# Performance work log

Hardware: AMD Instinct MI355X
Metric: run time of the kernel (lower is better)

## Reference

```python
import jax, jax.numpy as jnp
from jax import lax
import numpy as np

BN_EPS = 1e-3


def _bn_train(x, gamma, beta):
    # training-mode BatchNorm2d: batch stats over (N, H, W), biased variance
    mean = jnp.mean(x, axis=(0, 2, 3), keepdims=True)
    var = jnp.var(x, axis=(0, 2, 3), keepdims=True)
    g = gamma[None, :, None, None]
    b = beta[None, :, None, None]
    return (x - mean) * lax.rsqrt(var + BN_EPS) * g + b


def _pointwise(x, w, b, gamma, beta):
    # 1x1 conv + BN + relu (reluM = clamp(min=0))
    y = jnp.einsum('bchw,oc->bohw', x, w) + b[None, :, None, None]
    return jnp.maximum(_bn_train(y, gamma, beta), 0.0)


def _depthwise1d(x, w, b, gamma, beta):
    # depthwise (1,5) conv, zero pad width by 2 each side, BN, clamp(-8,8)
    C = w.shape[0]
    k = w[:, None, None, :]  # [C,1,1,5]
    y = lax.conv_general_dilated(
        x, k, window_strides=(1, 1), padding=[(0, 0), (2, 2)],
        feature_group_count=C,
        dimension_numbers=('NCHW', 'OIHW', 'NCHW'))
    y = y + b[None, :, None, None]
    return jnp.clip(_bn_train(y, gamma, beta), -8.0, 8.0)


def _iir(x, w3, gamma, beta):
    # y[0] = (a+b+c)*x[0];  y[r] = a*x[r] + b*x[r-1] + c*y[r-1]
    a = w3[0][:, None]  # w_curr_inp, [C,1]
    b = w3[1][:, None]  # w_prev_inp
    c = w3[2][:, None]  # w_prev_out
    xT = jnp.moveaxis(x, 2, 0)  # [H,B,C,W]
    y0 = (a + b + c) * xT[0]

    def step(y_prev, xs):
        x_curr, x_prev = xs
        y = a * x_curr + b * x_prev + c * y_prev
        return y, y

    _, ys = lax.scan(step, y0, (xT[1:], xT[:-1]))
    y = jnp.concatenate([y0[None], ys], axis=0)
    y = jnp.moveaxis(y, 0, 2)  # back to [B,C,H,W]
    return jnp.clip(_bn_train(y, gamma, beta), -8.0, 8.0)


def _process_unit(x, u, iir_w, iir_gamma, iir_beta, dw_w, dw_b, dw_gamma,
                  dw_beta, pw_w, pw_b, pw_gamma, pw_beta):
    h = _iir(x, iir_w[u], iir_gamma[u], iir_beta[u])
    h = _depthwise1d(h, dw_w[u], dw_b[u], dw_gamma[u], dw_beta[u])
    return _pointwise(h, pw_w[u], pw_b[u], pw_gamma[u], pw_beta[u])


def setup_inputs() -> dict:
    key = jax.random.key(0)
    ks = jax.random.split(key, 16)
    B, Cin, Cout, H, W = 4, 36, 72, 256, 256
    return {
        'x': jax.random.normal(ks[0], (B, Cin, H, W), jnp.float32),
        'expand_w': jax.random.normal(ks[1], (Cout, Cin), jnp.float32),
        'expand_b': jax.random.normal(ks[2], (Cout,), jnp.float32),
        'expand_gamma': jax.random.uniform(ks[3], (Cout,), jnp.float32),
        'expand_beta': jax.random.normal(ks[4], (Cout,), jnp.float32),
        'iir_w': jax.random.uniform(ks[5], (4, 3, Cout), jnp.float32),
        'iir_gamma': jax.random.uniform(ks[6], (4, Cout), jnp.float32),
        'iir_beta': jax.random.normal(ks[7], (4, Cout), jnp.float32),
        'dw_w': jax.random.normal(ks[8], (4, Cout, 5), jnp.float32),
        'dw_b': jax.random.normal(ks[9], (4, Cout), jnp.float32),
        'dw_gamma': jax.random.uniform(ks[10], (4, Cout), jnp.float32),
        'dw_beta': jax.random.normal(ks[11], (4, Cout), jnp.float32),
        'pw_w': jax.random.normal(ks[12], (4, Cout, Cout), jnp.float32),
        'pw_b': jax.random.normal(ks[13], (4, Cout), jnp.float32),
        'pw_gamma': jax.random.uniform(ks[14], (4, Cout), jnp.float32),
        'pw_beta': jax.random.normal(ks[15], (4, Cout), jnp.float32),
    }


def reference(x, expand_w, expand_b, expand_gamma, expand_beta, iir_w,
              iir_gamma, iir_beta, dw_w, dw_b, dw_gamma, dw_beta, pw_w,
              pw_b, pw_gamma, pw_beta):
    h = _pointwise(x, expand_w, expand_b, expand_gamma, expand_beta)
    unit = lambda z, u: _process_unit(z, u, iir_w, iir_gamma, iir_beta, dw_w,
                                      dw_b, dw_gamma, dw_beta, pw_w, pw_b,
                                      pw_gamma, pw_beta)
    h = h + unit(unit(h, 0), 1)
    h = h + unit(unit(h, 2), 3)
    return h
```

## Files before the change

### kernel.cpp

```cpp
#include <hip/hip_runtime.h>
#include <hip/hip_fp16.h>

#define BBATCH 4
#define CCH 72
#define HROW 256
#define WCOL 256
#define HWSZ (HROW*WCOL)
#define NPC (BBATCH*HROW*WCOL)
#define BNEPS 1e-3f
#define NSH 64
#define SST 144

typedef unsigned short u16;
typedef unsigned int u32;
typedef _Float16 h8 __attribute__((ext_vector_type(8)));
typedef float f32x4 __attribute__((ext_vector_type(4)));

__device__ __forceinline__ float h2f(u16 h_){ return __half2float(__ushort_as_half(h_)); }
__device__ __forceinline__ u16 f2h(float f){ return __half_as_ushort(__float2half(f)); }
__device__ __forceinline__ u32 pack2(float a, float b){ return (u32)f2h(a) | ((u32)f2h(b)<<16); }
__device__ __forceinline__ float clip8(float v){ return fminf(fmaxf(v,-8.f),8.f); }

__device__ __forceinline__ void get_ss_wave(int c, int lane, const float* __restrict__ pstat,
                                            const float* __restrict__ gam, const float* __restrict__ bet,
                                            float& sc, float& sh){
  float s = pstat[lane*SST + c];
  float q = pstat[lane*SST + 72 + c];
  #pragma unroll
  for (int off=32; off; off>>=1){ s += __shfl_xor(s,off); q += __shfl_xor(q,off); }
  float mean = s * (1.0f/(float)NPC);
  float var  = q * (1.0f/(float)NPC) - mean*mean;
  sc = gam[c] * rsqrtf(var + BNEPS);
  sh = bet[c] - mean*sc;
}

__global__ __launch_bounds__(256) void k_prep(const float* __restrict__ ew,
    const float* __restrict__ pwall, u16* __restrict__ Wp)
{
  for (int e = blockIdx.x*256 + threadIdx.x; e < 14*3200; e += gridDim.x*256){
    int slab = e / 3200, rem = e - slab*3200;
    int row = rem / 40, col = rem - row*40;
    float w = 0.f;
    if (slab < 2){
      int c = slab*32 + col;
      if (row < 72 && col < 32 && c < 36) w = ew[row*36 + c];
    } else {
      int u = (slab-2)/3, kb = (slab-2)%3;
      int c = kb*32 + col;
      if (row < 72 && col < 32) w = pwall[u*5184 + row*72 + c];
    }
    Wp[e] = f2h(w);
  }
}

template<int CIN, int RAW>
__global__ __launch_bounds__(512) void k_pw(const void* __restrict__ in_,
    u16* __restrict__ out, const u16* __restrict__ Wp,
    const float* __restrict__ pstat,
    const float* __restrict__ pgam, const float* __restrict__ pbet,
    float* __restrict__ ostat)
{
  constexpr int KB = (CIN + 31) / 32;
  __shared__ __align__(16) u16 xs[72*264];
  __shared__ float tsc[80], tsh[80];
  __shared__ float sst[72], sqt[72];
  float* pp4 = (float*)xs;
  float* pq4 = pp4 + 320;

  const int tid  = threadIdx.x;
  const int lane = tid & 63;
  const int wid  = tid >> 6;
  const int g    = lane >> 4;
  const int li   = lane & 15;
  const int b    = blockIdx.x >> 8;
  const int hrow = blockIdx.x & 255;

  if (tid < 72){ sst[tid] = 0.f; sqt[tid] = 0.f; }

  if constexpr (!RAW){
    int sg = tid >> 7, c = tid & 127;
    if (c < 72){
      float s = 0.f, q = 0.f;
      #pragma unroll
      for (int k2 = 0; k2 < 16; ++k2){
        s += pstat[(sg*16 + k2)*SST + c];
        q += pstat[(sg*16 + k2)*SST + 72 + c];
      }
      pp4[sg*80 + c] = s; pq4[sg*80 + c] = q;
    }
    __syncthreads();
    if (tid < CIN){
      float s = pp4[tid] + pp4[80+tid] + pp4[160+tid] + pp4[240+tid];
      float q = pq4[tid] + pq4[80+tid] + pq4[160+tid] + pq4[240+tid];
      float mean = s * (1.0f/(float)NPC);
      float var  = q * (1.0f/(float)NPC) - mean*mean;
      float scv  = pgam[tid] * rsqrtf(var + BNEPS);
      tsc[tid] = scv;
      tsh[tid] = pbet[tid] - mean*scv;
    }
    __syncthreads();
  }

  const size_t base_in = (size_t)b*CIN*HWSZ + (size_t)hrow*WCOL;
  const int px0 = wid*32 + li;
  f32x4 acc[5][2];
  #pragma unroll
  for (int mt=0; mt<5; ++mt){ acc[mt][0] = (f32x4){0,0,0,0}; acc[mt][1] = (f32x4){0,0,0,0}; }

  #pragma unroll
  for (int kb2 = 0; kb2 < KB; ++kb2){
    h8 bf0, bf1;
    #pragma unroll
    for (int j = 0; j < 8; ++j){
      int c  = kb2*32 + g*8 + j;
      int cc = (c < CIN) ? c : 0;
      float v0, v1;
      if constexpr (RAW){
        const float* ip = (const float*)in_ + base_in + (size_t)cc*HWSZ;
        v0 = ip[px0]; v1 = ip[px0 + 16];
      } else {
        const u16* ip = (const u16*)in_ + base_in + (size_t)cc*HWSZ;
        float scv = tsc[cc], shv = tsh[cc];
        v0 = clip8(h2f(ip[px0])*scv + shv);
        v1 = clip8(h2f(ip[px0 + 16])*scv + shv);
      }
      bool ok = (c < CIN);
      bf0[j] = (_Float16)(ok ? v0 : 0.f);
      bf1[j] = (_Float16)(ok ? v1 : 0.f);
    }
    #pragma unroll
    for (int mt = 0; mt < 5; ++mt){
      h8 ah = *(const h8*)(Wp + (size_t)(kb2*80 + mt*16 + li)*40 + g*8);
      acc[mt][0] = __builtin_amdgcn_mfma_f32_16x16x32_f16(ah, bf0, acc[mt][0], 0, 0, 0);
      acc[mt][1] = __builtin_amdgcn_mfma_f32_16x16x32_f16(ah, bf1, acc[mt][1], 0, 0, 0);
    }
  }

  #pragma unroll
  for (int mt = 0; mt < 5; ++mt){
    int o = mt*16 + g*4;
    if (o < 72){
      #pragma unroll
      for (int t2 = 0; t2 < 2; ++t2){
        int px = wid*32 + t2*16 + li;
        #pragma unroll
        for (int r = 0; r < 4; ++r)
          xs[(o + r)*264 + px] = f2h(acc[mt][t2][r]);
      }
    }
  }
  __syncthreads();

  #pragma unroll
  for (int it = 0; it < 5; ++it){
    int e = tid + it*512;
    if (e < 72*32){
      int o = e >> 5, m = e & 31;
      uint4 v = *(const uint4*)&xs[o*264 + m*8];
      u32 rr[4] = {v.x, v.y, v.z, v.w};
      float s = 0.f, q = 0.f;
      #pragma unroll
      for (int q2=0; q2<4; ++q2){
        float a  = h2f((u16)rr[q2]);
        float bq = h2f((u16)(rr[q2]>>16));
        s += a + bq;
        q = fmaf(a,a,q); q = fmaf(bq,bq,q);
      }
      *(uint4*)(out + (size_t)b*CCH*HWSZ + (size_t)o*HWSZ + (size_t)hrow*WCOL + m*8) = v;
      #pragma unroll
      for (int off = 1; off <= 16; off <<= 1){ s += __shfl_xor(s, off); q += __shfl_xor(q, off); }
      if ((lane & 31) == 0){ atomicAdd(&sst[o], s); atomicAdd(&sqt[o], q); }
    }
  }
  __syncthreads();
  if (tid < 72){
    float* oshard = ostat + (size_t)(blockIdx.x & (NSH-1))*SST;
    atomicAdd(oshard + tid,      sst[tid]);
    atomicAdd(oshard + 72 + tid, sqt[tid]);
  }
}

template<int MODE>
__global__ __launch_bounds__(256) void k_iir(const u16* __restrict__ in, u16* __restrict__ out,
    const float* __restrict__ wabc, u16* __restrict__ hbuf,
    const float* __restrict__ pstat,
    const float* __restrict__ pgam, const float* __restrict__ pbet,
    float* __restrict__ ostat)
{
  const int tid = threadIdx.x;
  const int bc = blockIdx.x;
  const int c = bc % CCH;
  float sc, sh; get_ss_wave(c, tid&63, pstat, pgam, pbet, sc, sh);
  const float ka = wabc[c], kb = wabc[CCH+c], kcc = wabc[2*CCH+c];
  const size_t base = (size_t)bc*HWSZ + tid;
  float xprev=0.f, yprev=0.f, lsum=0.f, lssq=0.f;

  float a0[16], a1[16], r0[16], r1[16];

  auto LOADC = [&](int hb, float* xv, float* rv){
    #pragma unroll
    for (int j=0;j<16;++j){
      size_t idx = base + (size_t)(hb+j)*WCOL;
      xv[j] = h2f(in[idx]);
      if (MODE==2) rv[j] = h2f(hbuf[idx]);
    }
  };
  auto COMPC = [&](int hb, const float* xv, const float* rv){
    float x[16];
    #pragma unroll
    for (int j=0;j<16;++j){
      float v = fmaxf(xv[j]*sc + sh, 0.f);
      if (MODE==1) hbuf[base + (size_t)(hb+j)*WCOL] = f2h(v);
      if (MODE==2){ v += rv[j]; hbuf[base + (size_t)(hb+j)*WCOL] = f2h(v); }
      x[j] = v;
    }
    if (hb == 0){ xprev = x[0]; yprev = x[0]; }
    float t[16];
    t[0] = fmaf(ka, x[0], kb*xprev);
    #pragma unroll
    for (int j=1;j<16;++j) t[j] = fmaf(ka, x[j], kb*x[j-1]);
    #pragma unroll
    for (int j=0;j<16;++j){
      yprev = fmaf(kcc, yprev, t[j]);
      out[base + (size_t)(hb+j)*WCOL] = f2h(yprev);
      lsum += yprev; lssq = fmaf(yprev,yprev,lssq);
    }
    xprev = x[15];
  };

  LOADC(0, a0, r0);
  #pragma unroll
  for (int hb = 0; hb < HROW; hb += 32){
    LOADC(hb+16, a1, r1);
    COMPC(hb, a0, r0);
    if (hb+32 < HROW) LOADC(hb+32, a0, r0);
    COMPC(hb+16, a1, r1);
  }

  #pragma unroll
  for (int off=32; off; off>>=1){ lsum += __shfl_xor(lsum,off); lssq += __shfl_xor(lssq,off); }
  __shared__ float rs[4], rq[4];
  if ((tid&63)==0){ rs[tid>>6]=lsum; rq[tid>>6]=lssq; }
  __syncthreads();
  if (tid==0){
    float* oshard = ostat + (size_t)(blockIdx.x & (NSH-1))*SST;
    atomicAdd(oshard + c,      rs[0]+rs[1]+rs[2]+rs[3]);
    atomicAdd(oshard + 72 + c, rq[0]+rq[1]+rq[2]+rq[3]);
  }
}

__global__ __launch_bounds__(256) void k_dw(const u16* __restrict__ in, u16* __restrict__ out,
    const float* __restrict__ wgt,
    const float* __restrict__ pstat,
    const float* __restrict__ pgam, const float* __restrict__ pbet,
    float* __restrict__ ostat)
{
  __shared__ float xs[8*264];
  __shared__ float rs[4], rq[4];
  const int tid = threadIdx.x;
  const int ht = blockIdx.x & 31;
  const int bc = blockIdx.x >> 5;
  const int c = bc % CCH;
  float sc, sh; get_ss_wave(c, tid&63, pstat, pgam, pbet, sc, sh);
  const float w0=wgt[c*5+0], w1=wgt[c*5+1], w2=wgt[c*5+2], w3=wgt[c*5+3], w4=wgt[c*5+4];
  const size_t base = (size_t)bc*HWSZ + (size_t)ht*(8*WCOL);

  if (tid < 64){
    int r = tid>>3, k = tid&7;
    xs[r*264 + (k<4 ? k : 256+k)] = 0.f;
  }
  const int r = tid >> 5, m = tid & 31;
  {
    uint4 v = *(const uint4*)(in + base + (size_t)r*WCOL + m*8);
    u32 rr[4] = {v.x, v.y, v.z, v.w};
    float f[8];
    #pragma unroll
    for (int q=0;q<4;++q){
      f[2*q]   = clip8(h2f((u16)rr[q])*sc + sh);
      f[2*q+1] = clip8(h2f((u16)(rr[q]>>16))*sc + sh);
    }
    float4* dst = (float4*)&xs[r*264 + 4 + m*8];
    dst[0] = make_float4(f[0],f[1],f[2],f[3]);
    dst[1] = make_float4(f[4],f[5],f[6],f[7]);
  }
  __syncthreads();
  float lsum=0.f, lssq=0.f;
  {
    const float* row = &xs[r*264 + m*8];
    float4 a0 = *(const float4*)(row+0);
    float4 a1 = *(const float4*)(row+4);
    float4 a2 = *(const float4*)(row+8);
    float4 a3 = *(const float4*)(row+12);
    float v[16] = {a0.x,a0.y,a0.z,a0.w, a1.x,a1.y,a1.z,a1.w,
                   a2.x,a2.y,a2.z,a2.w, a3.x,a3.y,a3.z,a3.w};
    float o[8];
    #pragma unroll
    for (int j=0;j<8;++j){
      float y = w0*v[j+2];
      y = fmaf(w1, v[j+3], y);
      y = fmaf(w2, v[j+4], y);
      y = fmaf(w3, v[j+5], y);
      y = fmaf(w4, v[j+6], y);
      o[j] = y;
      lsum += y; lssq = fmaf(y,y,lssq);
    }
    *(uint4*)(out + base + (size_t)r*WCOL + m*8) =
        make_uint4(pack2(o[0],o[1]), pack2(o[2],o[3]), pack2(o[4],o[5]), pack2(o[6],o[7]));
  }
  #pragma unroll
  for (int off=32; off; off>>=1){ lsum += __shfl_xor(lsum,off); lssq += __shfl_xor(lssq,off); }
  if ((tid&63)==0){ rs[tid>>6]=lsum; rq[tid>>6]=lssq; }
  __syncthreads();
  if (tid==0){
    float* oshard = ostat + (size_t)(blockIdx.x & (NSH-1))*SST;
    atomicAdd(oshard + c,      rs[0]+rs[1]+rs[2]+rs[3]);
    atomicAdd(oshard + 72 + c, rq[0]+rq[1]+rq[2]+rq[3]);
  }
}

__global__ __launch_bounds__(256) void k_final(const u16* __restrict__ y12, const u16* __restrict__ h1,
    float* __restrict__ outp,
    const float* __restrict__ pstat,
    const float* __restrict__ pgam, const float* __restrict__ pbet)
{
  __shared__ float tsc[CCH], tsh[CCH];
  if (threadIdx.x < CCH){
    int cc = threadIdx.x;
    float s=0.f, q=0.f;
    for (int sh2=0; sh2<NSH; ++sh2){ s += pstat[sh2*SST + cc]; q += pstat[sh2*SST + 72 + cc]; }
    float mean = s * (1.0f/(float)NPC);
    float var  = q * (1.0f/(float)NPC) - mean*mean;
    float scv = pgam[cc] * rsqrtf(var + BNEPS);
    tsc[cc] = scv;
    tsh[cc] = pbet[cc] - mean*scv;
  }
  __syncthreads();
  const size_t TOTALQ = (size_t)BBATCH*CCH*HWSZ/4;
  for (size_t q = (size_t)blockIdx.x*blockDim.x + threadIdx.x; q < TOTALQ;
       q += (size_t)gridDim.x*blockDim.x){
    int cch = (int)((q >> 14) % CCH);
    float sc = tsc[cch], sh = tsh[cch];
    uint2 a = *(const uint2*)(y12 + q*4);
    uint2 b = *(const uint2*)(h1 + q*4);
    float4 o;
    o.x = fmaxf(h2f((u16)a.x)*sc+sh, 0.f)       + h2f((u16)b.x);
    o.y = fmaxf(h2f((u16)(a.x>>16))*sc+sh, 0.f) + h2f((u16)(b.x>>16));
    o.z = fmaxf(h2f((u16)a.y)*sc+sh, 0.f)       + h2f((u16)b.y);
    o.w = fmaxf(h2f((u16)(a.y>>16))*sc+sh, 0.f) + h2f((u16)(b.y>>16));
    *(float4*)(outp + q*4) = o;
  }
}

extern "C" void kernel_launch(void* const* d_in, const int* in_sizes, int n_in,
                              void* d_out, int out_size, void* d_ws, size_t ws_size,
                              hipStream_t stream)
{
  (void)in_sizes; (void)n_in; (void)out_size;
  const float* x   = (const float*)d_in[0];
  const float* ew  = (const float*)d_in[1];
  const float* eg  = (const float*)d_in[3];
  const float* ebt = (const float*)d_in[4];
  const float* iw  = (const float*)d_in[5];
  const float* ig  = (const float*)d_in[6];
  const float* ibt = (const float*)d_in[7];
  const float* dwt = (const float*)d_in[8];
  const float* dg  = (const float*)d_in[10];
  const float* dbt = (const float*)d_in[11];
  const float* pw  = (const float*)d_in[12];
  const float* pg  = (const float*)d_in[14];
  const float* pbt = (const float*)d_in[15];
  float* outp = (float*)d_out;

  const size_t BUFE = (size_t)BBATCH*CCH*HWSZ;
  const size_t BUFB = BUFE*2;
  const size_t STATSB = (size_t)13*NSH*SST*sizeof(float);
  const size_t WPB = (size_t)14*3200*sizeof(u16);
  char* ws = (char*)d_ws;
  u16* A = (u16*)ws;
  u16* H = (u16*)(ws + BUFB);
  u16* B;
  float* stats;
  if (ws_size >= 3*BUFB + STATSB + WPB + 256){
    B = (u16*)(ws + 2*BUFB);
    stats = (float*)(ws + 3*BUFB);
  } else {
    B = (u16*)d_out;
    stats = (float*)(ws + 2*BUFB);
  }
  u16* Wp = (u16*)((char*)stats + STATSB);
  #define ST(s) (stats + (size_t)(s)*NSH*SST)
  #define WSLAB(u) (Wp + (size_t)(2 + 3*(u))*3200)

  hipMemsetAsync(stats, 0, STATSB, stream);

  dim3 blk(256);
  dim3 blkpw(512);
  k_prep<<<18, blk, 0, stream>>>(ew, pw, Wp);
  k_pw<36,1><<<BBATCH*HROW, blkpw, 0, stream>>>((const void*)x, A, Wp,
      nullptr, nullptr, nullptr, ST(0));
  k_iir<1><<<BBATCH*CCH, blk, 0, stream>>>(A, B, iw+0,   H, ST(0), eg, ebt, ST(1));
  k_dw    <<<BBATCH*CCH*32, blk, 0, stream>>>(B, A, dwt+0,    ST(1), ig+0,   ibt+0,   ST(2));
  k_pw<72,0><<<BBATCH*HROW, blkpw, 0, stream>>>(A, B, WSLAB(0), ST(2), dg+0,   dbt+0,   ST(3));
  k_iir<0><<<BBATCH*CCH, blk, 0, stream>>>(B, A, iw+216, nullptr, ST(3), pg+0,  pbt+0,  ST(4));
  k_dw    <<<BBATCH*CCH*32, blk, 0, stream>>>(A, B, dwt+360,  ST(4), ig+72,  ibt+72,  ST(5));
  k_pw<72,0><<<BBATCH*HROW, blkpw, 0, stream>>>(B, A, WSLAB(1), ST(5), dg+72,  dbt+72,  ST(6));
  k_iir<2><<<BBATCH*CCH, blk, 0, stream>>>(A, B, iw+432, H, ST(6), pg+72, pbt+72, ST(7));
  k_dw    <<<BBATCH*CCH*32, blk, 0, stream>>>(B, A, dwt+720,  ST(7), ig+144, ibt+144, ST(8));
  k_pw<72,0><<<BBATCH*HROW, blkpw, 0, stream>>>(A, B, WSLAB(2), ST(8), dg+144, dbt+144, ST(9));
  k_iir<0><<<BBATCH*CCH, blk, 0, stream>>>(B, A, iw+648, nullptr, ST(9), pg+144, pbt+144, ST(10));
  k_dw    <<<BBATCH*CCH*32, blk, 0, stream>>>(A, B, dwt+1080, ST(10), ig+216, ibt+216, ST(11));
  k_pw<72,0><<<BBATCH*HROW, blkpw, 0, stream>>>(B, A, WSLAB(3), ST(11), dg+216, dbt+216, ST(12));
  k_final<<<2048, blk, 0, stream>>>(A, H, outp, ST(12), pg+216, pbt+216);
  #undef ST
  #undef WSLAB
}
```

Before: 334.2 us.

## Split IIR into single-wave blocks and recompute expand output instead of storing it

The IIR kernel now launches four 64-thread blocks per (batch, channel), each covering 64 columns, instead of one 256-thread block. This gives four times as many blocks to fill the GPU and removes the shared-memory reduction and barrier. The first IIR no longer writes the post-BN expand activation to a separate buffer. A fourth workspace buffer keeps the raw expand output alive, and the MODE 2 IIR recomputes its BN+ReLU from the expand stats to form the residual, saving a full-tensor write. The cost is one more large workspace buffer and one more stats lookup in MODE 2.

```diff
diff --git a/kernel.cpp b/kernel.cpp
--- a/kernel.cpp
+++ b/kernel.cpp
@@ -181,18 +181,21 @@
 }
 
 template<int MODE>
-__global__ __launch_bounds__(256) void k_iir(const u16* __restrict__ in, u16* __restrict__ out,
-    const float* __restrict__ wabc, u16* __restrict__ hbuf,
-    const float* __restrict__ pstat,
-    const float* __restrict__ pgam, const float* __restrict__ pbet,
+__global__ __launch_bounds__(64) void k_iir(const u16* __restrict__ in, u16* __restrict__ out,
+    const float* __restrict__ wabc, u16* __restrict__ h1buf, const u16* __restrict__ in2,
+    const float* __restrict__ pstat, const float* __restrict__ pgam, const float* __restrict__ pbet,
+    const float* __restrict__ pstat2, const float* __restrict__ pgam2, const float* __restrict__ pbet2,
     float* __restrict__ ostat)
 {
   const int tid = threadIdx.x;
-  const int bc = blockIdx.x;
-  const int c = bc % CCH;
-  float sc, sh; get_ss_wave(c, tid&63, pstat, pgam, pbet, sc, sh);
+  const int wq  = blockIdx.x & 3;
+  const int bc  = blockIdx.x >> 2;
+  const int c   = bc % CCH;
+  float sc, sh; get_ss_wave(c, tid, pstat, pgam, pbet, sc, sh);
+  float sc2 = 0.f, sh2 = 0.f;
+  if (MODE==2) get_ss_wave(c, tid, pstat2, pgam2, pbet2, sc2, sh2);
   const float ka = wabc[c], kb = wabc[CCH+c], kcc = wabc[2*CCH+c];
-  const size_t base = (size_t)bc*HWSZ + tid;
+  const size_t base = (size_t)bc*HWSZ + wq*64 + tid;
   float xprev=0.f, yprev=0.f, lsum=0.f, lssq=0.f;
 
   float a0[16], a1[16], r0[16], r1[16];
@@ -202,7 +205,7 @@
     for (int j=0;j<16;++j){
       size_t idx = base + (size_t)(hb+j)*WCOL;
       xv[j] = h2f(in[idx]);
-      if (MODE==2) rv[j] = h2f(hbuf[idx]);
+      if (MODE==2) rv[j] = h2f(in2[idx]);
     }
   };
   auto COMPC = [&](int hb, const float* xv, const float* rv){
@@ -210,8 +213,10 @@
     #pragma unroll
     for (int j=0;j<16;++j){
       float v = fmaxf(xv[j]*sc + sh, 0.f);
-      if (MODE==1) hbuf[base + (size_t)(hb+j)*WCOL] = f2h(v);
-      if (MODE==2){ v += rv[j]; hbuf[base + (size_t)(hb+j)*WCOL] = f2h(v); }
+      if (MODE==2){
+        v += fmaxf(rv[j]*sc2 + sh2, 0.f);
+        h1buf[base + (size_t)(hb+j)*WCOL] = f2h(v);
+      }
       x[j] = v;
     }
     if (hb == 0){ xprev = x[0]; yprev = x[0]; }
@@ -239,13 +244,10 @@
 
   #pragma unroll
   for (int off=32; off; off>>=1){ lsum += __shfl_xor(lsum,off); lssq += __shfl_xor(lssq,off); }
-  __shared__ float rs[4], rq[4];
-  if ((tid&63)==0){ rs[tid>>6]=lsum; rq[tid>>6]=lssq; }
-  __syncthreads();
   if (tid==0){
     float* oshard = ostat + (size_t)(blockIdx.x & (NSH-1))*SST;
-    atomicAdd(oshard + c,      rs[0]+rs[1]+rs[2]+rs[3]);
-    atomicAdd(oshard + 72 + c, rq[0]+rq[1]+rq[2]+rq[3]);
+    atomicAdd(oshard + c,      lsum);
+    atomicAdd(oshard + 72 + c, lssq);
   }
 }
 
@@ -377,17 +379,16 @@
   const size_t WPB = (size_t)14*3200*sizeof(u16);
   char* ws = (char*)d_ws;
   u16* A = (u16*)ws;
-  u16* H = (u16*)(ws + BUFB);
+  u16* C = (u16*)(ws + BUFB);
+  u16* H = (u16*)(ws + 2*BUFB);
+  float* stats = (float*)(ws + 3*BUFB);
+  u16* Wp = (u16*)((char*)stats + STATSB);
   u16* B;
-  float* stats;
-  if (ws_size >= 3*BUFB + STATSB + WPB + 256){
-    B = (u16*)(ws + 2*BUFB);
-    stats = (float*)(ws + 3*BUFB);
+  if (ws_size >= 4*BUFB + STATSB + WPB + 256){
+    B = (u16*)((char*)Wp + ((WPB+255)&~(size_t)255));
   } else {
     B = (u16*)d_out;
-    stats = (float*)(ws + 2*BUFB);
-  }
-  u16* Wp = (u16*)((char*)stats + STATSB);
+  }
   #define ST(s) (stats + (size_t)(s)*NSH*SST)
   #define WSLAB(u) (Wp + (size_t)(2 + 3*(u))*3200)
 
@@ -395,22 +396,28 @@
 
   dim3 blk(256);
   dim3 blkpw(512);
+  dim3 blkiir(64);
+  const int GIIR = BBATCH*CCH*4;
   k_prep<<<18, blk, 0, stream>>>(ew, pw, Wp);
   k_pw<36,1><<<BBATCH*HROW, blkpw, 0, stream>>>((const void*)x, A, Wp,
       nullptr, nullptr, nullptr, ST(0));
-  k_iir<1><<<BBATCH*CCH, blk, 0, stream>>>(A, B, iw+0,   H, ST(0), eg, ebt, ST(1));
-  k_dw    <<<BBATCH*CCH*32, blk, 0, stream>>>(B, A, dwt+0,    ST(1), ig+0,   ibt+0,   ST(2));
-  k_pw<72,0><<<BBATCH*HROW, blkpw, 0, stream>>>(A, B, WSLAB(0), ST(2), dg+0,   dbt+0,   ST(3));
-  k_iir<0><<<BBATCH*CCH, blk, 0, stream>>>(B, A, iw+216, nullptr, ST(3), pg+0,  pbt+0,  ST(4));
-  k_dw    <<<BBATCH*CCH*32, blk, 0, stream>>>(A, B, dwt+360,  ST(4), ig+72,  ibt+72,  ST(5));
-  k_pw<72,0><<<BBATCH*HROW, blkpw, 0, stream>>>(B, A, WSLAB(1), ST(5), dg+72,  dbt+72,  ST(6));
-  k_iir<2><<<BBATCH*CCH, blk, 0, stream>>>(A, B, iw+432, H, ST(6), pg+72, pbt+72, ST(7));
-  k_dw    <<<BBATCH*CCH*32, blk, 0, stream>>>(B, A, dwt+720,  ST(7), ig+144, ibt+144, ST(8));
-  k_pw<72,0><<<BBATCH*HROW, blkpw, 0, stream>>>(A, B, WSLAB(2), ST(8), dg+144, dbt+144, ST(9));
-  k_iir<0><<<BBATCH*CCH, blk, 0, stream>>>(B, A, iw+648, nullptr, ST(9), pg+144, pbt+144, ST(10));
-  k_dw    <<<BBATCH*CCH*32, blk, 0, stream>>>(A, B, dwt+1080, ST(10), ig+216, ibt+216, ST(11));
-  k_pw<72,0><<<BBATCH*HROW, blkpw, 0, stream>>>(B, A, WSLAB(3), ST(11), dg+216, dbt+216, ST(12));
-  k_final<<<2048, blk, 0, stream>>>(A, H, outp, ST(12), pg+216, pbt+216);
+  k_iir<0><<<GIIR, blkiir, 0, stream>>>(A, B, iw+0, nullptr, nullptr,
+      ST(0), eg, ebt, nullptr, nullptr, nullptr, ST(1));
+  k_dw    <<<BBATCH*CCH*32, blk, 0, stream>>>(B, C, dwt+0,    ST(1), ig+0,   ibt+0,   ST(2));
+  k_pw<72,0><<<BBATCH*HROW, blkpw, 0, stream>>>(C, B, WSLAB(0), ST(2), dg+0,   dbt+0,   ST(3));
+  k_iir<0><<<GIIR, blkiir, 0, stream>>>(B, C, iw+216, nullptr, nullptr,
+      ST(3), pg+0, pbt+0, nullptr, nullptr, nullptr, ST(4));
+  k_dw    <<<BBATCH*CCH*32, blk, 0, stream>>>(C, B, dwt+360,  ST(4), ig+72,  ibt+72,  ST(5));
+  k_pw<72,0><<<BBATCH*HROW, blkpw, 0, stream>>>(B, C, WSLAB(1), ST(5), dg+72,  dbt+72,  ST(6));
+  k_iir<2><<<GIIR, blkiir, 0, stream>>>(C, B, iw+432, H, A,
+      ST(6), pg+72, pbt+72, ST(0), eg, ebt, ST(7));
+  k_dw    <<<BBATCH*CCH*32, blk, 0, stream>>>(B, C, dwt+720,  ST(7), ig+144, ibt+144, ST(8));
+  k_pw<72,0><<<BBATCH*HROW, blkpw, 0, stream>>>(C, B, WSLAB(2), ST(8), dg+144, dbt+144, ST(9));
+  k_iir<0><<<GIIR, blkiir, 0, stream>>>(B, C, iw+648, nullptr, nullptr,
+      ST(9), pg+144, pbt+144, nullptr, nullptr, nullptr, ST(10));
+  k_dw    <<<BBATCH*CCH*32, blk, 0, stream>>>(C, B, dwt+1080, ST(10), ig+216, ibt+216, ST(11));
+  k_pw<72,0><<<BBATCH*HROW, blkpw, 0, stream>>>(B, C, WSLAB(3), ST(11), dg+216, dbt+216, ST(12));
+  k_final<<<2048, blk, 0, stream>>>(C, H, outp, ST(12), pg+216, pbt+216);
   #undef ST
   #undef WSLAB
 }
```

Measured after the change: 321.3 us (median of 2 runs). 3.8% less time.
